# Kernel optimization log

Hardware: AMD Instinct MI355X
Metric: run time of the kernel (lower is better)

The kernel has to match this reference:

```python
import jax, jax.numpy as jnp
import numpy as np

N = 1_000_000   # gaussians
K_NB = 10       # neighbor control points per gaussian
K_TOTAL = 300   # num_fine control points


def _normalize(q, eps=1e-8):
    return q / jnp.maximum(jnp.linalg.norm(q, axis=-1, keepdims=True), eps)


def quaternion_to_rotation_matrix(q):
    # q: [..., 4] in (w, x, y, z); normalized before conversion
    q = _normalize(q)
    w, x, y, z = q[..., 0], q[..., 1], q[..., 2], q[..., 3]
    R = jnp.stack([
        jnp.stack([1 - 2 * (y * y + z * z), 2 * (x * y - w * z), 2 * (x * z + w * y)], axis=-1),
        jnp.stack([2 * (x * y + w * z), 1 - 2 * (x * x + z * z), 2 * (y * z - w * x)], axis=-1),
        jnp.stack([2 * (x * z - w * y), 2 * (y * z + w * x), 1 - 2 * (x * x + y * y)], axis=-1),
    ], axis=-2)  # [..., 3, 3]
    return R


def quaternion_multiply(a, b):
    # Hamilton product, (w, x, y, z)
    aw, ax, ay, az = a[..., 0], a[..., 1], a[..., 2], a[..., 3]
    bw, bx, by, bz = b[..., 0], b[..., 1], b[..., 2], b[..., 3]
    return jnp.stack([
        aw * bw - ax * bx - ay * by - az * bz,
        aw * bx + ax * bw + ay * bz - az * by,
        aw * by - ax * bz + ay * bw + az * bx,
        aw * bz + ax * by - ay * bx + az * bw,
    ], axis=-1)


def setup_inputs() -> dict:
    key = jax.random.key(0)
    ks = jax.random.split(key, 7)
    means = jax.random.normal(ks[0], (N, 3), dtype=jnp.float32)
    quaternions = _normalize(jax.random.normal(ks[1], (N, 4), dtype=jnp.float32))
    w = jax.random.uniform(ks[2], (N, K_NB), dtype=jnp.float32) + 1e-3
    weights = w / w.sum(-1, keepdims=True)  # blending weights sum to 1
    indices = jax.random.randint(ks[3], (N, K_NB), 0, K_TOTAL)
    ctrl_translations = 0.1 * jax.random.normal(ks[4], (K_TOTAL, 3), dtype=jnp.float32)
    ctrl_rotations = _normalize(jax.random.normal(ks[5], (K_TOTAL, 4), dtype=jnp.float32))
    ctrl_positions = jax.random.normal(ks[6], (K_TOTAL, 3), dtype=jnp.float32)
    return {
        'means': means, 'quaternions': quaternions, 'weights': weights,
        'ctrl_translations': ctrl_translations, 'ctrl_rotations': ctrl_rotations,
        'ctrl_positions': ctrl_positions, 'indices': indices,
    }


def reference(means, quaternions, weights, ctrl_translations, ctrl_rotations, ctrl_positions, indices):
    # gather neighbor control-point transforms
    nb_trans = ctrl_translations[indices]   # [N, K, 3]
    nb_rots = ctrl_rotations[indices]       # [N, K, 4]
    nb_pos = ctrl_positions[indices]        # [N, K, 3]

    diff = means[:, None, :] - nb_pos                       # [N, K, 3]
    R_ctrl = quaternion_to_rotation_matrix(nb_rots)         # [N, K, 3, 3]
    rotated_diff = jnp.einsum('nkij,nkj->nki', R_ctrl, diff)
    deformed_per_cp = rotated_diff + nb_pos + nb_trans      # [N, K, 3]

    w = weights[..., None]                                  # [N, K, 1]
    deformed_means = (w * deformed_per_cp).sum(axis=1)      # [N, 3]

    blended_rot = _normalize((w * nb_rots).sum(axis=1))     # [N, 4]
    deformed_quats = quaternion_multiply(blended_rot, quaternions)
    return deformed_means, deformed_quats
```

## Files before the change

kernel.cpp:

```cpp
#include <hip/hip_runtime.h>
#include <math.h>


template <int KNB>
__global__ __launch_bounds__(256) void deform_kernel(
    const float* __restrict__ means,
    const float* __restrict__ quats,
    const float* __restrict__ weights,
    const float* __restrict__ ctrl_trans,
    const float* __restrict__ ctrl_rot,
    const float* __restrict__ ctrl_pos,
    const int*   __restrict__ indices,
    float* __restrict__ out_means,
    float* __restrict__ out_quats,
    int N, int K_TOTAL)
{
    extern __shared__ float4 s4[];

    for (int cp = threadIdx.x; cp < K_TOTAL; cp += blockDim.x) {
        float qw = ctrl_rot[cp * 4 + 0];
        float qx = ctrl_rot[cp * 4 + 1];
        float qy = ctrl_rot[cp * 4 + 2];
        float qz = ctrl_rot[cp * 4 + 3];
        float n  = sqrtf(qw * qw + qx * qx + qy * qy + qz * qz);
        float inv = 1.0f / fmaxf(n, 1e-8f);
        float w = qw * inv, x = qx * inv, y = qy * inv, z = qz * inv;
        float R00 = 1.0f - 2.0f * (y * y + z * z);
        float R01 = 2.0f * (x * y - w * z);
        float R02 = 2.0f * (x * z + w * y);
        float R10 = 2.0f * (x * y + w * z);
        float R11 = 1.0f - 2.0f * (x * x + z * z);
        float R12 = 2.0f * (y * z - w * x);
        float R20 = 2.0f * (x * z - w * y);
        float R21 = 2.0f * (y * z + w * x);
        float R22 = 1.0f - 2.0f * (x * x + y * y);
        float px = ctrl_pos[cp * 3 + 0];
        float py = ctrl_pos[cp * 3 + 1];
        float pz = ctrl_pos[cp * 3 + 2];
        float tx = ctrl_trans[cp * 3 + 0];
        float ty = ctrl_trans[cp * 3 + 1];
        float tz = ctrl_trans[cp * 3 + 2];
        float bx = px + tx - (R00 * px + R01 * py + R02 * pz);
        float by = py + ty - (R10 * px + R11 * py + R12 * pz);
        float bz = pz + tz - (R20 * px + R21 * py + R22 * pz);
        s4[cp * 5 + 0] = make_float4(R00, R01, R02, R10);
        s4[cp * 5 + 1] = make_float4(R11, R12, R20, R21);
        s4[cp * 5 + 2] = make_float4(R22, bx, by, bz);
        s4[cp * 5 + 3] = make_float4(qw, qx, qy, qz);
    }
    __syncthreads();

    int i = blockIdx.x * blockDim.x + threadIdx.x;
    if (i >= N) return;

    const int*   idx_row = indices + (long long)i * KNB;
    const float* w_row   = weights + (long long)i * KNB;

    float acc[16];
#pragma unroll
    for (int j = 0; j < 16; j++) acc[j] = 0.0f;

#pragma unroll
    for (int k = 0; k < KNB; k++) {
        int   cp = idx_row[k];
        float w  = w_row[k];
        float4 a = s4[cp * 5 + 0];
        float4 b = s4[cp * 5 + 1];
        float4 c = s4[cp * 5 + 2];
        float4 d = s4[cp * 5 + 3];
        acc[0]  = fmaf(w, a.x, acc[0]);
        acc[1]  = fmaf(w, a.y, acc[1]);
        acc[2]  = fmaf(w, a.z, acc[2]);
        acc[3]  = fmaf(w, a.w, acc[3]);
        acc[4]  = fmaf(w, b.x, acc[4]);
        acc[5]  = fmaf(w, b.y, acc[5]);
        acc[6]  = fmaf(w, b.z, acc[6]);
        acc[7]  = fmaf(w, b.w, acc[7]);
        acc[8]  = fmaf(w, c.x, acc[8]);
        acc[9]  = fmaf(w, c.y, acc[9]);
        acc[10] = fmaf(w, c.z, acc[10]);
        acc[11] = fmaf(w, c.w, acc[11]);
        acc[12] = fmaf(w, d.x, acc[12]);
        acc[13] = fmaf(w, d.y, acc[13]);
        acc[14] = fmaf(w, d.z, acc[14]);
        acc[15] = fmaf(w, d.w, acc[15]);
    }

    float mx = means[i * 3 + 0];
    float my = means[i * 3 + 1];
    float mz = means[i * 3 + 2];

    float dmx = acc[0] * mx + acc[1] * my + acc[2] * mz + acc[9];
    float dmy = acc[3] * mx + acc[4] * my + acc[5] * mz + acc[10];
    float dmz = acc[6] * mx + acc[7] * my + acc[8] * mz + acc[11];

    out_means[i * 3 + 0] = dmx;
    out_means[i * 3 + 1] = dmy;
    out_means[i * 3 + 2] = dmz;

    float bw = acc[12], bx = acc[13], by = acc[14], bz = acc[15];
    float n  = sqrtf(bw * bw + bx * bx + by * by + bz * bz);
    float inv = 1.0f / fmaxf(n, 1e-8f);
    bw *= inv; bx *= inv; by *= inv; bz *= inv;

    float4 g = ((const float4*)quats)[i];
    float gw = g.x, gx = g.y, gy = g.z, gz = g.w;

    float ow = bw * gw - bx * gx - by * gy - bz * gz;
    float ox = bw * gx + bx * gw + by * gz - bz * gy;
    float oy = bw * gy - bx * gz + by * gw + bz * gx;
    float oz = bw * gz + bx * gy - by * gx + bz * gw;

    float4* oq = (float4*)(out_quats + (long long)i * 4);
    *oq = make_float4(ow, ox, oy, oz);
}

__global__ __launch_bounds__(256) void deform_kernel_generic(
    const float* __restrict__ means,
    const float* __restrict__ quats,
    const float* __restrict__ weights,
    const float* __restrict__ ctrl_trans,
    const float* __restrict__ ctrl_rot,
    const float* __restrict__ ctrl_pos,
    const int*   __restrict__ indices,
    float* __restrict__ out_means,
    float* __restrict__ out_quats,
    int N, int K_NB, int K_TOTAL)
{
    extern __shared__ float4 s4[];
    for (int cp = threadIdx.x; cp < K_TOTAL; cp += blockDim.x) {
        float qw = ctrl_rot[cp * 4 + 0];
        float qx = ctrl_rot[cp * 4 + 1];
        float qy = ctrl_rot[cp * 4 + 2];
        float qz = ctrl_rot[cp * 4 + 3];
        float n  = sqrtf(qw * qw + qx * qx + qy * qy + qz * qz);
        float inv = 1.0f / fmaxf(n, 1e-8f);
        float w = qw * inv, x = qx * inv, y = qy * inv, z = qz * inv;
        float R00 = 1.0f - 2.0f * (y * y + z * z);
        float R01 = 2.0f * (x * y - w * z);
        float R02 = 2.0f * (x * z + w * y);
        float R10 = 2.0f * (x * y + w * z);
        float R11 = 1.0f - 2.0f * (x * x + z * z);
        float R12 = 2.0f * (y * z - w * x);
        float R20 = 2.0f * (x * z - w * y);
        float R21 = 2.0f * (y * z + w * x);
        float R22 = 1.0f - 2.0f * (x * x + y * y);
        float px = ctrl_pos[cp * 3 + 0];
        float py = ctrl_pos[cp * 3 + 1];
        float pz = ctrl_pos[cp * 3 + 2];
        float tx = ctrl_trans[cp * 3 + 0];
        float ty = ctrl_trans[cp * 3 + 1];
        float tz = ctrl_trans[cp * 3 + 2];
        float bx = px + tx - (R00 * px + R01 * py + R02 * pz);
        float by = py + ty - (R10 * px + R11 * py + R12 * pz);
        float bz = pz + tz - (R20 * px + R21 * py + R22 * pz);
        s4[cp * 5 + 0] = make_float4(R00, R01, R02, R10);
        s4[cp * 5 + 1] = make_float4(R11, R12, R20, R21);
        s4[cp * 5 + 2] = make_float4(R22, bx, by, bz);
        s4[cp * 5 + 3] = make_float4(qw, qx, qy, qz);
    }
    __syncthreads();

    int i = blockIdx.x * blockDim.x + threadIdx.x;
    if (i >= N) return;

    const int*   idx_row = indices + (long long)i * K_NB;
    const float* w_row   = weights + (long long)i * K_NB;

    float acc[16];
#pragma unroll
    for (int j = 0; j < 16; j++) acc[j] = 0.0f;

    for (int k = 0; k < K_NB; k++) {
        int   cp = idx_row[k];
        float w  = w_row[k];
        float4 a = s4[cp * 5 + 0];
        float4 b = s4[cp * 5 + 1];
        float4 c = s4[cp * 5 + 2];
        float4 d = s4[cp * 5 + 3];
        acc[0]  = fmaf(w, a.x, acc[0]);
        acc[1]  = fmaf(w, a.y, acc[1]);
        acc[2]  = fmaf(w, a.z, acc[2]);
        acc[3]  = fmaf(w, a.w, acc[3]);
        acc[4]  = fmaf(w, b.x, acc[4]);
        acc[5]  = fmaf(w, b.y, acc[5]);
        acc[6]  = fmaf(w, b.z, acc[6]);
        acc[7]  = fmaf(w, b.w, acc[7]);
        acc[8]  = fmaf(w, c.x, acc[8]);
        acc[9]  = fmaf(w, c.y, acc[9]);
        acc[10] = fmaf(w, c.z, acc[10]);
        acc[11] = fmaf(w, c.w, acc[11]);
        acc[12] = fmaf(w, d.x, acc[12]);
        acc[13] = fmaf(w, d.y, acc[13]);
        acc[14] = fmaf(w, d.z, acc[14]);
        acc[15] = fmaf(w, d.w, acc[15]);
    }

    float mx = means[i * 3 + 0];
    float my = means[i * 3 + 1];
    float mz = means[i * 3 + 2];

    float dmx = acc[0] * mx + acc[1] * my + acc[2] * mz + acc[9];
    float dmy = acc[3] * mx + acc[4] * my + acc[5] * mz + acc[10];
    float dmz = acc[6] * mx + acc[7] * my + acc[8] * mz + acc[11];

    out_means[i * 3 + 0] = dmx;
    out_means[i * 3 + 1] = dmy;
    out_means[i * 3 + 2] = dmz;

    float bw = acc[12], bx = acc[13], by = acc[14], bz = acc[15];
    float n  = sqrtf(bw * bw + bx * bx + by * by + bz * bz);
    float inv = 1.0f / fmaxf(n, 1e-8f);
    bw *= inv; bx *= inv; by *= inv; bz *= inv;

    float4 g = ((const float4*)quats)[i];
    float gw = g.x, gx = g.y, gy = g.z, gz = g.w;

    float ow = bw * gw - bx * gx - by * gy - bz * gz;
    float ox = bw * gx + bx * gw + by * gz - bz * gy;
    float oy = bw * gy - bx * gz + by * gw + bz * gx;
    float oz = bw * gz + bx * gy - by * gx + bz * gw;

    float4* oq = (float4*)(out_quats + (long long)i * 4);
    *oq = make_float4(ow, ox, oy, oz);
}

extern "C" void kernel_launch(void* const* d_in, const int* in_sizes, int n_in,
                              void* d_out, int out_size, void* d_ws, size_t ws_size,
                              hipStream_t stream) {
    const float* means      = (const float*)d_in[0];
    const float* quats      = (const float*)d_in[1];
    const float* weights    = (const float*)d_in[2];
    const float* ctrl_trans = (const float*)d_in[3];
    const float* ctrl_rot   = (const float*)d_in[4];
    const float* ctrl_pos   = (const float*)d_in[5];
    const int*   indices    = (const int*)d_in[6];

    int N       = in_sizes[0] / 3;
    int K_NB    = in_sizes[2] / N;
    int K_TOTAL = in_sizes[3] / 3;

    float* out_means = (float*)d_out;
    float* out_quats = (float*)d_out + (long long)N * 3;

    int block = 256;
    int grid  = (N + block - 1) / block;
    size_t smem = (size_t)K_TOTAL * 5 * sizeof(float4);

    if (K_NB == 10) {
        deform_kernel<10><<<grid, block, smem, stream>>>(
            means, quats, weights, ctrl_trans, ctrl_rot, ctrl_pos, indices,
            out_means, out_quats, N, K_TOTAL);
    } else {
        deform_kernel_generic<<<grid, block, smem, stream>>>(
            means, quats, weights, ctrl_trans, ctrl_rot, ctrl_pos, indices,
            out_means, out_quats, N, K_NB, K_TOTAL);
    }
}
```

Measured before the change: 147.9 us.

## Blend quaternion outer products and precompute control-point table in a separate kernel

Each control point is now stored as a normalized quaternion plus a translation offset (two float4 instead of five), and the per-gaussian loop accumulates weighted quaternion second moments instead of full rotation matrices. The blended 3x3 matrix is rebuilt once per gaussian from those moments. When a workspace buffer is available, a small separate kernel builds the table once and each block copies it into LDS instead of recomputing rotations per block. This cuts LDS traffic and per-block setup, at the cost of an extra kernel launch and a dependence on workspace being provided.

```diff
diff --git a/kernel.cpp b/kernel.cpp
--- a/kernel.cpp
+++ b/kernel.cpp
@@ -2,8 +2,158 @@
 #include <math.h>
 
 
+__device__ __forceinline__ void compute_cp(
+    const float* __restrict__ ctrl_trans,
+    const float* __restrict__ ctrl_rot,
+    const float* __restrict__ ctrl_pos,
+    int cp, float4* q_out, float4* b_out)
+{
+    float qw = ctrl_rot[cp * 4 + 0];
+    float qx = ctrl_rot[cp * 4 + 1];
+    float qy = ctrl_rot[cp * 4 + 2];
+    float qz = ctrl_rot[cp * 4 + 3];
+    float n   = sqrtf(qw * qw + qx * qx + qy * qy + qz * qz);
+    float inv = 1.0f / fmaxf(n, 1e-8f);
+    float w = qw * inv, x = qx * inv, y = qy * inv, z = qz * inv;
+    float R00 = 1.0f - 2.0f * (y * y + z * z);
+    float R01 = 2.0f * (x * y - w * z);
+    float R02 = 2.0f * (x * z + w * y);
+    float R10 = 2.0f * (x * y + w * z);
+    float R11 = 1.0f - 2.0f * (x * x + z * z);
+    float R12 = 2.0f * (y * z - w * x);
+    float R20 = 2.0f * (x * z - w * y);
+    float R21 = 2.0f * (y * z + w * x);
+    float R22 = 1.0f - 2.0f * (x * x + y * y);
+    float px = ctrl_pos[cp * 3 + 0];
+    float py = ctrl_pos[cp * 3 + 1];
+    float pz = ctrl_pos[cp * 3 + 2];
+    float tx = ctrl_trans[cp * 3 + 0];
+    float ty = ctrl_trans[cp * 3 + 1];
+    float tz = ctrl_trans[cp * 3 + 2];
+    *q_out = make_float4(w, x, y, z);
+    *b_out = make_float4(px + tx - (R00 * px + R01 * py + R02 * pz),
+                         py + ty - (R10 * px + R11 * py + R12 * pz),
+                         pz + tz - (R20 * px + R21 * py + R22 * pz),
+                         0.0f);
+}
+
+__global__ __launch_bounds__(256) void build_table_kernel(
+    const float* __restrict__ ctrl_trans,
+    const float* __restrict__ ctrl_rot,
+    const float* __restrict__ ctrl_pos,
+    float4* __restrict__ table, int K_TOTAL)
+{
+    int cp = blockIdx.x * blockDim.x + threadIdx.x;
+    if (cp >= K_TOTAL) return;
+    float4 q, b;
+    compute_cp(ctrl_trans, ctrl_rot, ctrl_pos, cp, &q, &b);
+    table[cp] = q;
+    table[K_TOTAL + cp] = b;
+}
+
+template <int KNB>
+__device__ __forceinline__ void deform_body(
+    const float4* __restrict__ s4,
+    const float* __restrict__ means,
+    const float* __restrict__ quats,
+    const float* __restrict__ weights,
+    const int*   __restrict__ indices,
+    float* __restrict__ out_means,
+    float* __restrict__ out_quats,
+    int i, int K_TOTAL, int K_NB_rt)
+{
+    const int kn = (KNB > 0) ? KNB : K_NB_rt;
+    const int*   idx_row = indices + (long long)i * kn;
+    const float* w_row   = weights + (long long)i * kn;
+
+    float W = 0.0f;
+    float Mxx = 0.0f, Myy = 0.0f, Mzz = 0.0f;
+    float Mxy = 0.0f, Mxz = 0.0f, Myz = 0.0f;
+    float Mwx = 0.0f, Mwy = 0.0f, Mwz = 0.0f;
+    float qsw = 0.0f, qsx = 0.0f, qsy = 0.0f, qsz = 0.0f;
+    float bsx = 0.0f, bsy = 0.0f, bsz = 0.0f;
+
+#pragma unroll
+    for (int k = 0; k < kn; k++) {
+        int   cp = idx_row[k];
+        float w  = w_row[k];
+        float4 q = s4[cp];
+        float4 b = s4[K_TOTAL + cp];
+        float tw = w * q.x, tx = w * q.y, ty = w * q.z, tz = w * q.w;
+        W += w;
+        Mxx = fmaf(tx, q.y, Mxx);
+        Myy = fmaf(ty, q.z, Myy);
+        Mzz = fmaf(tz, q.w, Mzz);
+        Mxy = fmaf(tx, q.z, Mxy);
+        Mxz = fmaf(tx, q.w, Mxz);
+        Myz = fmaf(ty, q.w, Myz);
+        Mwx = fmaf(tw, q.y, Mwx);
+        Mwy = fmaf(tw, q.z, Mwy);
+        Mwz = fmaf(tw, q.w, Mwz);
+        qsw += tw; qsx += tx; qsy += ty; qsz += tz;
+        bsx = fmaf(w, b.x, bsx);
+        bsy = fmaf(w, b.y, bsy);
+        bsz = fmaf(w, b.z, bsz);
+    }
+
+    float mx = means[i * 3 + 0];
+    float my = means[i * 3 + 1];
+    float mz = means[i * 3 + 2];
+
+    float A00 = W - 2.0f * (Myy + Mzz);
+    float A01 = 2.0f * (Mxy - Mwz);
+    float A02 = 2.0f * (Mxz + Mwy);
+    float A10 = 2.0f * (Mxy + Mwz);
+    float A11 = W - 2.0f * (Mxx + Mzz);
+    float A12 = 2.0f * (Myz - Mwx);
+    float A20 = 2.0f * (Mxz - Mwy);
+    float A21 = 2.0f * (Myz + Mwx);
+    float A22 = W - 2.0f * (Mxx + Myy);
+
+    out_means[i * 3 + 0] = fmaf(A00, mx, fmaf(A01, my, fmaf(A02, mz, bsx)));
+    out_means[i * 3 + 1] = fmaf(A10, mx, fmaf(A11, my, fmaf(A12, mz, bsy)));
+    out_means[i * 3 + 2] = fmaf(A20, mx, fmaf(A21, my, fmaf(A22, mz, bsz)));
+
+    float n   = sqrtf(qsw * qsw + qsx * qsx + qsy * qsy + qsz * qsz);
+    float inv = 1.0f / fmaxf(n, 1e-8f);
+    float bw = qsw * inv, bx = qsx * inv, by = qsy * inv, bz = qsz * inv;
+
+    float4 g = ((const float4*)quats)[i];
+    float gw = g.x, gx = g.y, gy = g.z, gz = g.w;
+
+    float ow = bw * gw - bx * gx - by * gy - bz * gz;
+    float ox = bw * gx + bx * gw + by * gz - bz * gy;
+    float oy = bw * gy - bx * gz + by * gw + bz * gx;
+    float oz = bw * gz + bx * gy - by * gx + bz * gw;
+
+    float4* oq = (float4*)(out_quats + (long long)i * 4);
+    *oq = make_float4(ow, ox, oy, oz);
+}
+
 template <int KNB>
 __global__ __launch_bounds__(256) void deform_kernel(
+    const float* __restrict__ means,
+    const float* __restrict__ quats,
+    const float* __restrict__ weights,
+    const float4* __restrict__ table,
+    const int*   __restrict__ indices,
+    float* __restrict__ out_means,
+    float* __restrict__ out_quats,
+    int N, int K_TOTAL, int K_NB_rt)
+{
+    extern __shared__ float4 s4[];
+    int nelem = 2 * K_TOTAL;
+    for (int t = threadIdx.x; t < nelem; t += blockDim.x) s4[t] = table[t];
+    __syncthreads();
+
+    int i = blockIdx.x * blockDim.x + threadIdx.x;
+    if (i >= N) return;
+    deform_body<KNB>(s4, means, quats, weights, indices, out_means, out_quats,
+                     i, K_TOTAL, K_NB_rt);
+}
+
+template <int KNB>
+__global__ __launch_bounds__(256) void deform_fused_kernel(
     const float* __restrict__ means,
     const float* __restrict__ quats,
     const float* __restrict__ weights,
@@ -13,216 +163,21 @@
     const int*   __restrict__ indices,
     float* __restrict__ out_means,
     float* __restrict__ out_quats,
-    int N, int K_TOTAL)
+    int N, int K_TOTAL, int K_NB_rt)
 {
     extern __shared__ float4 s4[];
-
     for (int cp = threadIdx.x; cp < K_TOTAL; cp += blockDim.x) {
-        float qw = ctrl_rot[cp * 4 + 0];
-        float qx = ctrl_rot[cp * 4 + 1];
-        float qy = ctrl_rot[cp * 4 + 2];
-        float qz = ctrl_rot[cp * 4 + 3];
-        float n  = sqrtf(qw * qw + qx * qx + qy * qy + qz * qz);
-        float inv = 1.0f / fmaxf(n, 1e-8f);
-        float w = qw * inv, x = qx * inv, y = qy * inv, z = qz * inv;
-        float R00 = 1.0f - 2.0f * (y * y + z * z);
-        float R01 = 2.0f * (x * y - w * z);
-        float R02 = 2.0f * (x * z + w * y);
-        float R10 = 2.0f * (x * y + w * z);
-        float R11 = 1.0f - 2.0f * (x * x + z * z);
-        float R12 = 2.0f * (y * z - w * x);
-        float R20 = 2.0f * (x * z - w * y);
-        float R21 = 2.0f * (y * z + w * x);
-        float R22 = 1.0f - 2.0f * (x * x + y * y);
-        float px = ctrl_pos[cp * 3 + 0];
-        float py = ctrl_pos[cp * 3 + 1];
-        float pz = ctrl_pos[cp * 3 + 2];
-        float tx = ctrl_trans[cp * 3 + 0];
-        float ty = ctrl_trans[cp * 3 + 1];
-        float tz = ctrl_trans[cp * 3 + 2];
-        float bx = px + tx - (R00 * px + R01 * py + R02 * pz);
-        float by = py + ty - (R10 * px + R11 * py + R12 * pz);
-        float bz = pz + tz - (R20 * px + R21 * py + R22 * pz);
-        s4[cp * 5 + 0] = make_float4(R00, R01, R02, R10);
-        s4[cp * 5 + 1] = make_float4(R11, R12, R20, R21);
-        s4[cp * 5 + 2] = make_float4(R22, bx, by, bz);
-        s4[cp * 5 + 3] = make_float4(qw, qx, qy, qz);
+        float4 q, b;
+        compute_cp(ctrl_trans, ctrl_rot, ctrl_pos, cp, &q, &b);
+        s4[cp] = q;
+        s4[K_TOTAL + cp] = b;
     }
     __syncthreads();
 
     int i = blockIdx.x * blockDim.x + threadIdx.x;
     if (i >= N) return;
-
-    const int*   idx_row = indices + (long long)i * KNB;
-    const float* w_row   = weights + (long long)i * KNB;
-
-    float acc[16];
-#pragma unroll
-    for (int j = 0; j < 16; j++) acc[j] = 0.0f;
-
-#pragma unroll
-    for (int k = 0; k < KNB; k++) {
-        int   cp = idx_row[k];
-        float w  = w_row[k];
-        float4 a = s4[cp * 5 + 0];
-        float4 b = s4[cp * 5 + 1];
-        float4 c = s4[cp * 5 + 2];
-        float4 d = s4[cp * 5 + 3];
-        acc[0]  = fmaf(w, a.x, acc[0]);
-        acc[1]  = fmaf(w, a.y, acc[1]);
-        acc[2]  = fmaf(w, a.z, acc[2]);
-        acc[3]  = fmaf(w, a.w, acc[3]);
-        acc[4]  = fmaf(w, b.x, acc[4]);
-        acc[5]  = fmaf(w, b.y, acc[5]);
-        acc[6]  = fmaf(w, b.z, acc[6]);
-        acc[7]  = fmaf(w, b.w, acc[7]);
-        acc[8]  = fmaf(w, c.x, acc[8]);
-        acc[9]  = fmaf(w, c.y, acc[9]);
-        acc[10] = fmaf(w, c.z, acc[10]);
-        acc[11] = fmaf(w, c.w, acc[11]);
-        acc[12] = fmaf(w, d.x, acc[12]);
-        acc[13] = fmaf(w, d.y, acc[13]);
-        acc[14] = fmaf(w, d.z, acc[14]);
-        acc[15] = fmaf(w, d.w, acc[15]);
-    }
-
-    float mx = means[i * 3 + 0];
-    float my = means[i * 3 + 1];
-    float mz = means[i * 3 + 2];
-
-    float dmx = acc[0] * mx + acc[1] * my + acc[2] * mz + acc[9];
-    float dmy = acc[3] * mx + acc[4] * my + acc[5] * mz + acc[10];
-    float dmz = acc[6] * mx + acc[7] * my + acc[8] * mz + acc[11];
-
-    out_means[i * 3 + 0] = dmx;
-    out_means[i * 3 + 1] = dmy;
-    out_means[i * 3 + 2] = dmz;
-
-    float bw = acc[12], bx = acc[13], by = acc[14], bz = acc[15];
-    float n  = sqrtf(bw * bw + bx * bx + by * by + bz * bz);
-    float inv = 1.0f / fmaxf(n, 1e-8f);
-    bw *= inv; bx *= inv; by *= inv; bz *= inv;
-
-    float4 g = ((const float4*)quats)[i];
-    float gw = g.x, gx = g.y, gy = g.z, gz = g.w;
-
-    float ow = bw * gw - bx * gx - by * gy - bz * gz;
-    float ox = bw * gx + bx * gw + by * gz - bz * gy;
-    float oy = bw * gy - bx * gz + by * gw + bz * gx;
-    float oz = bw * gz + bx * gy - by * gx + bz * gw;
-
-    float4* oq = (float4*)(out_quats + (long long)i * 4);
-    *oq = make_float4(ow, ox, oy, oz);
-}
-
-__global__ __launch_bounds__(256) void deform_kernel_generic(
-    const float* __restrict__ means,
-    const float* __restrict__ quats,
-    const float* __restrict__ weights,
-    const float* __restrict__ ctrl_trans,
-    const float* __restrict__ ctrl_rot,
-    const float* __restrict__ ctrl_pos,
-    const int*   __restrict__ indices,
-    float* __restrict__ out_means,
-    float* __restrict__ out_quats,
-    int N, int K_NB, int K_TOTAL)
-{
-    extern __shared__ float4 s4[];
-    for (int cp = threadIdx.x; cp < K_TOTAL; cp += blockDim.x) {
-        float qw = ctrl_rot[cp * 4 + 0];
-        float qx = ctrl_rot[cp * 4 + 1];
-        float qy = ctrl_rot[cp * 4 + 2];
-        float qz = ctrl_rot[cp * 4 + 3];
-        float n  = sqrtf(qw * qw + qx * qx + qy * qy + qz * qz);
-        float inv = 1.0f / fmaxf(n, 1e-8f);
-        float w = qw * inv, x = qx * inv, y = qy * inv, z = qz * inv;
-        float R00 = 1.0f - 2.0f * (y * y + z * z);
-        float R01 = 2.0f * (x * y - w * z);
-        float R02 = 2.0f * (x * z + w * y);
-        float R10 = 2.0f * (x * y + w * z);
-        float R11 = 1.0f - 2.0f * (x * x + z * z);
-        float R12 = 2.0f * (y * z - w * x);
-        float R20 = 2.0f * (x * z - w * y);
-        float R21 = 2.0f * (y * z + w * x);
-        float R22 = 1.0f - 2.0f * (x * x + y * y);
-        float px = ctrl_pos[cp * 3 + 0];
-        float py = ctrl_pos[cp * 3 + 1];
-        float pz = ctrl_pos[cp * 3 + 2];
-        float tx = ctrl_trans[cp * 3 + 0];
-        float ty = ctrl_trans[cp * 3 + 1];
-        float tz = ctrl_trans[cp * 3 + 2];
-        float bx = px + tx - (R00 * px + R01 * py + R02 * pz);
-        float by = py + ty - (R10 * px + R11 * py + R12 * pz);
-        float bz = pz + tz - (R20 * px + R21 * py + R22 * pz);
-        s4[cp * 5 + 0] = make_float4(R00, R01, R02, R10);
-        s4[cp * 5 + 1] = make_float4(R11, R12, R20, R21);
-        s4[cp * 5 + 2] = make_float4(R22, bx, by, bz);
-        s4[cp * 5 + 3] = make_float4(qw, qx, qy, qz);
-    }
-    __syncthreads();
-
-    int i = blockIdx.x * blockDim.x + threadIdx.x;
-    if (i >= N) return;
-
-    const int*   idx_row = indices + (long long)i * K_NB;
-    const float* w_row   = weights + (long long)i * K_NB;
-
-    float acc[16];
-#pragma unroll
-    for (int j = 0; j < 16; j++) acc[j] = 0.0f;
-
-    for (int k = 0; k < K_NB; k++) {
-        int   cp = idx_row[k];
-        float w  = w_row[k];
-        float4 a = s4[cp * 5 + 0];
-        float4 b = s4[cp * 5 + 1];
-        float4 c = s4[cp * 5 + 2];
-        float4 d = s4[cp * 5 + 3];
-        acc[0]  = fmaf(w, a.x, acc[0]);
-        acc[1]  = fmaf(w, a.y, acc[1]);
-        acc[2]  = fmaf(w, a.z, acc[2]);
-        acc[3]  = fmaf(w, a.w, acc[3]);
-        acc[4]  = fmaf(w, b.x, acc[4]);
-        acc[5]  = fmaf(w, b.y, acc[5]);
-        acc[6]  = fmaf(w, b.z, acc[6]);
-        acc[7]  = fmaf(w, b.w, acc[7]);
-        acc[8]  = fmaf(w, c.x, acc[8]);
-        acc[9]  = fmaf(w, c.y, acc[9]);
-        acc[10] = fmaf(w, c.z, acc[10]);
-        acc[11] = fmaf(w, c.w, acc[11]);
-        acc[12] = fmaf(w, d.x, acc[12]);
-        acc[13] = fmaf(w, d.y, acc[13]);
-        acc[14] = fmaf(w, d.z, acc[14]);
-        acc[15] = fmaf(w, d.w, acc[15]);
-    }
-
-    float mx = means[i * 3 + 0];
-    float my = means[i * 3 + 1];
-    float mz = means[i * 3 + 2];
-
-    float dmx = acc[0] * mx + acc[1] * my + acc[2] * mz + acc[9];
-    float dmy = acc[3] * mx + acc[4] * my + acc[5] * mz + acc[10];
-    float dmz = acc[6] * mx + acc[7] * my + acc[8] * mz + acc[11];
-
-    out_means[i * 3 + 0] = dmx;
-    out_means[i * 3 + 1] = dmy;
-    out_means[i * 3 + 2] = dmz;
-
-    float bw = acc[12], bx = acc[13], by = acc[14], bz = acc[15];
-    float n  = sqrtf(bw * bw + bx * bx + by * by + bz * bz);
-    float inv = 1.0f / fmaxf(n, 1e-8f);
-    bw *= inv; bx *= inv; by *= inv; bz *= inv;
-
-    float4 g = ((const float4*)quats)[i];
-    float gw = g.x, gx = g.y, gy = g.z, gz = g.w;
-
-    float ow = bw * gw - bx * gx - by * gy - bz * gz;
-    float ox = bw * gx + bx * gw + by * gz - bz * gy;
-    float oy = bw * gy - bx * gz + by * gw + bz * gx;
-    float oz = bw * gz + bx * gy - by * gx + bz * gw;
-
-    float4* oq = (float4*)(out_quats + (long long)i * 4);
-    *oq = make_float4(ow, ox, oy, oz);
+    deform_body<KNB>(s4, means, quats, weights, indices, out_means, out_quats,
+                     i, K_TOTAL, K_NB_rt);
 }
 
 extern "C" void kernel_launch(void* const* d_in, const int* in_sizes, int n_in,
@@ -245,15 +200,31 @@
 
     int block = 256;
     int grid  = (N + block - 1) / block;
-    size_t smem = (size_t)K_TOTAL * 5 * sizeof(float4);
-
-    if (K_NB == 10) {
-        deform_kernel<10><<<grid, block, smem, stream>>>(
-            means, quats, weights, ctrl_trans, ctrl_rot, ctrl_pos, indices,
-            out_means, out_quats, N, K_TOTAL);
+    size_t tbl_bytes = (size_t)K_TOTAL * 2 * sizeof(float4);
+    size_t smem = tbl_bytes;
+
+    if (d_ws != nullptr && ws_size >= tbl_bytes) {
+        int gb = (K_TOTAL + block - 1) / block;
+        build_table_kernel<<<gb, block, 0, stream>>>(
+            ctrl_trans, ctrl_rot, ctrl_pos, (float4*)d_ws, K_TOTAL);
+        if (K_NB == 10) {
+            deform_kernel<10><<<grid, block, smem, stream>>>(
+                means, quats, weights, (const float4*)d_ws, indices,
+                out_means, out_quats, N, K_TOTAL, K_NB);
+        } else {
+            deform_kernel<0><<<grid, block, smem, stream>>>(
+                means, quats, weights, (const float4*)d_ws, indices,
+                out_means, out_quats, N, K_TOTAL, K_NB);
+        }
     } else {
-        deform_kernel_generic<<<grid, block, smem, stream>>>(
-            means, quats, weights, ctrl_trans, ctrl_rot, ctrl_pos, indices,
-            out_means, out_quats, N, K_NB, K_TOTAL);
+        if (K_NB == 10) {
+            deform_fused_kernel<10><<<grid, block, smem, stream>>>(
+                means, quats, weights, ctrl_trans, ctrl_rot, ctrl_pos, indices,
+                out_means, out_quats, N, K_TOTAL, K_NB);
+        } else {
+            deform_fused_kernel<0><<<grid, block, smem, stream>>>(
+                means, quats, weights, ctrl_trans, ctrl_rot, ctrl_pos, indices,
+                out_means, out_quats, N, K_TOTAL, K_NB);
+        }
     }
 }
```

Measured after the change: 147.8 us. About the same (-0.1%).
